# Kernel tuning notes

Hardware: AMD Instinct MI355X
Metric: run time of the kernel (lower is better)

Reference implementation:

```python
import jax, jax.numpy as jnp
import numpy as np

B, T, V, C = 4, 2048, 1024, 256
NB_L, NB_M, NB_H = 16, 32, 64


def _band_w(basis, coeffs, soft):
    # basis: (V, 2*nb), coeffs: (C, 2*nb) -> w: (V, C)
    w = basis @ coeffs.T
    return jax.nn.softmax(w, axis=0) if soft else w


def _rms_norm(x):
    eps = jnp.asarray(jnp.finfo(x.dtype).eps, x.dtype)
    return x * jax.lax.rsqrt(jnp.mean(jnp.square(x), axis=-1, keepdims=True) + eps)


def _retrieve(x, basis, qc, kc, vc, decay_logit):
    # x: (B,T,V) -> (B,T,C); decay-weighted dense T x T retrieval
    q = x @ _band_w(basis, qc, True)
    k = x @ _band_w(basis, kc, True)
    v = x @ _band_w(basis, vc, True)
    scores = jnp.einsum('btc,bsc->bts', q, k)
    decay = jax.nn.sigmoid(decay_logit)
    pos = jnp.arange(T)
    diff = pos[None, :] - pos[:, None]  # diff[i,j] = j - i (as in torch code)
    dw = (decay ** jnp.maximum(diff - 1, 0).astype(x.dtype)) * (diff > 0).astype(x.dtype)
    return jnp.einsum('bts,bsc->btc', scores * dw[None], v)


def _project(r, basis, oc, out_scale):
    return jnp.einsum('btc,vc->btv', r, basis @ oc.T) * out_scale


def _transform(x, basis, read_c, mix, bias):
    z = x @ _band_w(basis, read_c, True)
    return jax.nn.gelu(z @ mix + bias, approximate=False)


def _write_back(h, basis, write_c, out_scale):
    return jnp.einsum('btc,vc->btv', h, basis @ write_c.T) * out_scale


def setup_inputs() -> dict:
    key = jax.random.key(0)
    ks = iter(jax.random.split(key, 48))
    s = 0.02

    def rn(shape, scale=s):
        return jax.random.normal(next(ks), shape, dtype=jnp.float32) * scale

    d = {
        'x': jax.random.normal(next(ks), (B, T, V), dtype=jnp.float32),
        'basis_low': jax.random.normal(next(ks), (V, 2 * NB_L), dtype=jnp.float32),
        'basis_mid': jax.random.normal(next(ks), (V, 2 * NB_M), dtype=jnp.float32),
        'basis_high': jax.random.normal(next(ks), (V, 2 * NB_H), dtype=jnp.float32),
    }
    for pre, nb, dec in (('slow', NB_L, 4.0), ('fast', NB_H, 2.0)):
        for nm in ('q', 'k', 'v', 'o'):
            d[f'{pre}_{nm}'] = rn((C, 2 * nb))
        d[f'{pre}_decay'] = jnp.asarray(dec, jnp.float32)
        d[f'{pre}_scale'] = jnp.asarray(0.1, jnp.float32)
    for pre, nb in (('low', NB_L), ('mid', NB_M), ('high', NB_H)):
        d[f'{pre}_read'] = rn((C, 2 * nb))
        d[f'{pre}_write'] = rn((C, 2 * nb))
        d[f'{pre}_mix'] = rn((C, C))
        d[f'{pre}_bias'] = jnp.zeros((C,), jnp.float32)
        d[f'{pre}_oscale'] = jnp.asarray(0.1, jnp.float32)
    d['tg_w'] = rn((C, C)); d['tg_b'] = jnp.zeros((C,), jnp.float32)
    d['alpha_w'] = rn((C, C)); d['alpha_b'] = jnp.zeros((C,), jnp.float32)
    for nm in ('mem_slow_scale', 'mem_fast_scale', 'op_low_scale', 'op_mid_scale', 'op_high_scale'):
        d[nm] = jnp.ones((1,), jnp.float32)
    return d


def reference(x, basis_low, basis_mid, basis_high,
              slow_q, slow_k, slow_v, slow_o, slow_decay, slow_scale,
              fast_q, fast_k, fast_v, fast_o, fast_decay, fast_scale,
              low_read, low_write, low_mix, low_bias, low_oscale,
              mid_read, mid_write, mid_mix, mid_bias, mid_oscale,
              high_read, high_write, high_mix, high_bias, high_oscale,
              tg_w, tg_b, alpha_w, alpha_b,
              mem_slow_scale, mem_fast_scale, op_low_scale, op_mid_scale, op_high_scale):
    # Phase 1: temporal mixing
    xn = _rms_norm(x)
    r_slow = _retrieve(xn, basis_low, slow_q, slow_k, slow_v, slow_decay)
    r_fast = _retrieve(xn, basis_high, fast_q, fast_k, fast_v, fast_decay)
    tg = jax.nn.sigmoid(r_slow @ tg_w + tg_b)
    r_fast = tg * r_fast
    x = x + (_project(r_slow, basis_low, slow_o, slow_scale) * mem_slow_scale
             + _project(r_fast, basis_high, fast_o, fast_scale) * mem_fast_scale)
    # Phase 2: band processing
    xn = _rms_norm(x)
    h_low = _transform(xn, basis_low, low_read, low_mix, low_bias)
    h_mid = _transform(xn, basis_mid, mid_read, mid_mix, mid_bias)
    h_high = _transform(xn, basis_high, high_read, high_mix, high_bias)
    ag = jax.nn.sigmoid(h_low @ alpha_w + alpha_b)
    h_high = ag * h_high
    x = x + (_write_back(h_low, basis_low, low_write, low_oscale) * op_low_scale
             + _write_back(h_mid, basis_mid, mid_write, mid_oscale) * op_mid_scale
             + _write_back(h_high, basis_high, high_write, high_oscale) * op_high_scale)
    return x
```

## Files before the change

kernel.cpp:

```cpp
#include <hip/hip_runtime.h>
#include <math.h>

#define BB 4
#define TT 2048
#define VV 1024
#define CC 256
#define MR (BB*TT)

using short8  = __attribute__((ext_vector_type(8))) short;
using ushort8 = __attribute__((ext_vector_type(8))) unsigned short;
using f32x4   = __attribute__((ext_vector_type(4))) float;

__device__ __forceinline__ float bs2f(unsigned short s) {
    return __uint_as_float(((unsigned int)s) << 16);
}
__device__ __forceinline__ unsigned short f2bs(float f) {
    unsigned int u = __float_as_uint(f);
    u += 0x7fffu + ((u >> 16) & 1u);
    return (unsigned short)(u >> 16);
}
__device__ __forceinline__ void gl_lds16(const void* g, void* l) {
    __builtin_amdgcn_global_load_lds(
        (const __attribute__((address_space(1))) unsigned int*)g,
        (__attribute__((address_space(3))) unsigned int*)l, 16, 0, 0);
}
__device__ __forceinline__ float sigm(float x) { return 1.f / (1.f + expf(-x)); }
__device__ __forceinline__ float erf_f(float x) {
    float ax = fabsf(x);
    float t = 1.f / (1.f + 0.3275911f * ax);
    float p = t * (0.254829592f + t * (-0.284496736f + t * (1.421413741f +
              t * (-1.453152027f + t * 1.061405429f))));
    float e = 1.f - p * expf(-ax * ax);
    return copysignf(e, x);
}

struct CastJob { const float* src; unsigned short* dst; int n; };
struct CastArgs { CastJob j[17]; };

__global__ void cast_bf16_multi(CastArgs a) {
    CastJob jb = a.j[blockIdx.x];
    int off = (blockIdx.y * 256 + threadIdx.x) * 8;
    if (off + 8 > jb.n) return;
    float4 v0 = *reinterpret_cast<const float4*>(jb.src + off);
    float4 v1 = *reinterpret_cast<const float4*>(jb.src + off + 4);
    ushort8 u;
    u[0] = f2bs(v0.x); u[1] = f2bs(v0.y); u[2] = f2bs(v0.z); u[3] = f2bs(v0.w);
    u[4] = f2bs(v1.x); u[5] = f2bs(v1.y); u[6] = f2bs(v1.z); u[7] = f2bs(v1.w);
    *reinterpret_cast<ushort8*>(jb.dst + off) = u;
}

__global__ void softmax_rows(unsigned short* __restrict__ w) {
    int row = blockIdx.x * 4 + (threadIdx.x >> 6);
    int lane = threadIdx.x & 63;
    ushort4* rp = reinterpret_cast<ushort4*>(w + (size_t)row * 1024);
    float v[16];
    #pragma unroll
    for (int i = 0; i < 4; ++i) {
        ushort4 u = rp[lane + i * 64];
        v[i*4+0] = bs2f(u.x); v[i*4+1] = bs2f(u.y);
        v[i*4+2] = bs2f(u.z); v[i*4+3] = bs2f(u.w);
    }
    float m = v[0];
    #pragma unroll
    for (int i = 1; i < 16; ++i) m = fmaxf(m, v[i]);
    #pragma unroll
    for (int o = 32; o > 0; o >>= 1) m = fmaxf(m, __shfl_xor(m, o));
    float s = 0.f;
    #pragma unroll
    for (int i = 0; i < 16; ++i) { v[i] = expf(v[i] - m); s += v[i]; }
    #pragma unroll
    for (int o = 32; o > 0; o >>= 1) s += __shfl_xor(s, o);
    float inv = 1.f / s;
    #pragma unroll
    for (int i = 0; i < 4; ++i) {
        ushort4 u;
        u.x = f2bs(v[i*4+0] * inv); u.y = f2bs(v[i*4+1] * inv);
        u.z = f2bs(v[i*4+2] * inv); u.w = f2bs(v[i*4+3] * inv);
        rp[lane + i * 64] = u;
    }
}

__global__ void prep_T5(const float* s0, const float* s1, const float* s2,
                        const float* s3, const float* s4,
                        unsigned short* d0, unsigned short* d1, unsigned short* d2,
                        unsigned short* d3, unsigned short* d4) {
    int y = blockIdx.y;
    const float* W = y == 0 ? s0 : y == 1 ? s1 : y == 2 ? s2 : y == 3 ? s3 : s4;
    unsigned short* WT = y == 0 ? d0 : y == 1 ? d1 : y == 2 ? d2 : y == 3 ? d3 : d4;
    int n = blockIdx.x, k = threadIdx.x;
    WT[(size_t)n * 256 + k] = f2bs(W[(size_t)k * 256 + n]);
}

__global__ void rmsnorm_k(const float* __restrict__ x, unsigned short* __restrict__ xn) {
    int row = blockIdx.x * 4 + (threadIdx.x >> 6);
    int lane = threadIdx.x & 63;
    const float4* src = reinterpret_cast<const float4*>(x + (size_t)row * VV);
    float4 v[4];
    float s = 0.f;
    #pragma unroll
    for (int i = 0; i < 4; ++i) {
        v[i] = src[lane + i * 64];
        s += v[i].x*v[i].x + v[i].y*v[i].y + v[i].z*v[i].z + v[i].w*v[i].w;
    }
    #pragma unroll
    for (int o = 32; o > 0; o >>= 1) s += __shfl_xor(s, o);
    float r = rsqrtf(s * (1.f / VV) + 1.1920929e-7f);
    ushort4* dst = reinterpret_cast<ushort4*>(xn + (size_t)row * VV);
    #pragma unroll
    for (int i = 0; i < 4; ++i) {
        ushort4 u;
        u.x = f2bs(v[i].x * r); u.y = f2bs(v[i].y * r);
        u.z = f2bs(v[i].z * r); u.w = f2bs(v[i].w * r);
        dst[lane + i * 64] = u;
    }
}

__global__ void transpose4_k(const unsigned short* __restrict__ qkv,
                             unsigned short* __restrict__ vt_s,
                             unsigned short* __restrict__ vt_f,
                             unsigned short* __restrict__ kts_s,
                             unsigned short* __restrict__ kts_f,
                             const float* __restrict__ dls,
                             const float* __restrict__ dlf) {
    __shared__ unsigned short tile[32][33];
    int z = blockIdx.z, b = z & 3, which = z >> 2;
    int srcoff = which == 0 ? 512 : which == 1 ? 1280 : which == 2 ? 256 : 1024;
    unsigned short* dst = which == 0 ? vt_s : which == 1 ? vt_f : which == 2 ? kts_s : kts_f;
    float l2d = 0.f;
    if (which == 2) l2d = log2f(sigm(dls[0]));
    if (which == 3) l2d = log2f(sigm(dlf[0]));
    int t0 = blockIdx.x * 32, c0 = blockIdx.y * 32;
    int tx = threadIdx.x & 31, ty = threadIdx.x >> 5;
    const unsigned short* src = qkv + srcoff;
    #pragma unroll
    for (int i = 0; i < 4; ++i) {
        int r = ty + i * 8;
        tile[r][tx] = src[(size_t)(b * TT + t0 + r) * 1536 + c0 + tx];
    }
    __syncthreads();
    float w = (which >= 2) ? exp2f(l2d * (float)((t0 + tx) & 127)) : 1.f;
    #pragma unroll
    for (int i = 0; i < 4; ++i) {
        int r = ty + i * 8;
        dst[((size_t)b * CC + c0 + r) * TT + t0 + tx] = f2bs(bs2f(tile[tx][r]) * w);
    }
}

__device__ __forceinline__ void gemm64_core(
    const unsigned short* A, int lda, const unsigned short* Bt, int ldb,
    int K, int m0, int n0, short8* As, short8* Bs, f32x4 (&acc)[2][2]) {
    const int tid = threadIdx.x;
    const int lane = tid & 63, wid = tid >> 6;
    const int wm = wid >> 1, wn = wid & 1;
    const int lrow = tid >> 2, lch = tid & 3;
    const int sws = lch ^ ((lrow >> 1) & 3);
    const unsigned short* ag = A + (size_t)(m0 + lrow) * lda + lch * 8;
    const unsigned short* bg = Bt + (size_t)(n0 + lrow) * ldb + lch * 8;
    #pragma unroll
    for (int i = 0; i < 2; ++i)
        #pragma unroll
        for (int j = 0; j < 2; ++j) acc[i][j] = {0.f, 0.f, 0.f, 0.f};
    const int g = lane >> 4;
    const int ra0 = wm * 32 + (lane & 15);
    const int rb0 = wn * 32 + (lane & 15);
    for (int k0 = 0; k0 < K; k0 += 32) {
        As[lrow * 4 + sws] = *reinterpret_cast<const short8*>(ag + k0);
        Bs[lrow * 4 + sws] = *reinterpret_cast<const short8*>(bg + k0);
        __syncthreads();
        short8 af[2], bf[2];
        #pragma unroll
        for (int i = 0; i < 2; ++i) {
            int ra = ra0 + i * 16;
            af[i] = As[ra * 4 + (g ^ ((ra >> 1) & 3))];
            int rb = rb0 + i * 16;
            bf[i] = Bs[rb * 4 + (g ^ ((rb >> 1) & 3))];
        }
        #pragma unroll
        for (int i = 0; i < 2; ++i)
            #pragma unroll
            for (int j = 0; j < 2; ++j)
                acc[i][j] = __builtin_amdgcn_mfma_f32_16x16x32_bf16(af[i], bf[j], acc[i][j], 0, 0, 0);
        __syncthreads();
    }
}

#define EPI_LOOP(MV, NV, VV_, BODY)                                            \
    {   const int lane_ = threadIdx.x & 63, wid_ = threadIdx.x >> 6;           \
        const int wm_ = wid_ >> 1, wn_ = wid_ & 1;                             \
        _Pragma("unroll")                                                      \
        for (int i_ = 0; i_ < 2; ++i_)                                         \
        { _Pragma("unroll")                                                    \
          for (int j_ = 0; j_ < 2; ++j_)                                       \
          { _Pragma("unroll")                                                  \
            for (int r_ = 0; r_ < 4; ++r_)                                     \
            { int MV = m0 + wm_ * 32 + i_ * 16 + (lane_ >> 4) * 4 + r_;        \
              int NV = n0 + wn_ * 32 + j_ * 16 + (lane_ & 15);                 \
              float VV_ = acc[i_][j_][r_];                                     \
              BODY } } } }

struct MJob {
    const unsigned short* A; const unsigned short* Bt; unsigned short* outb;
    const float* s1; const float* s2;
    int lda, ldb, K, ldo, gx, nblk;
};
struct MJobs5 { MJob j[5]; };

template<int EPI>
__global__ __launch_bounds__(256)
void gemm_multi_k(MJobs5 js) {
    int bid = blockIdx.x, ji = 0, base = 0;
    while (bid >= base + js.j[ji].nblk) { base += js.j[ji].nblk; ++ji; }
    MJob jb = js.j[ji];
    int rem = bid - base;
    int m0 = (rem / jb.gx) * 64, n0 = (rem % jb.gx) * 64;
    __shared__ short8 As[256], Bs[256];
    f32x4 acc[2][2];
    gemm64_core(jb.A, jb.lda, jb.Bt, jb.ldb, jb.K, m0, n0, As, Bs, acc);
    float sc = 1.f;
    if constexpr (EPI == 4) sc = jb.s1[0] * jb.s2[0];
    EPI_LOOP(m, n, v, { jb.outb[(size_t)m * jb.ldo + n] = f2bs(v * sc); })
}

__global__ __launch_bounds__(256)
void sig_k(const unsigned short* A, int lda, const unsigned short* Bt,
           const float* bias, const unsigned short* aux, int ldaux,
           unsigned short* outb, int ldo, int coloff) {
    int m0 = blockIdx.y * 64, n0 = blockIdx.x * 64;
    __shared__ short8 As[256], Bs[256];
    f32x4 acc[2][2];
    gemm64_core(A, lda, Bt, 256, 256, m0, n0, As, Bs, acc);
    EPI_LOOP(m, n, v, {
        float s = sigm(v + bias[n]);
        float a = bs2f(aux[(size_t)m * ldaux + n]);
        outb[(size_t)m * ldo + coloff + n] = f2bs(s * a);
    })
}

__global__ __launch_bounds__(256)
void gelu3_k(const unsigned short* zbuf, const unsigned short* WT_mix,
             const float* lb, const float* mb, const float* hb,
             unsigned short* hcat, unsigned short* hhigh) {
    int zi = blockIdx.z;
    const unsigned short* A = zbuf + zi * 256;
    const unsigned short* Bt = WT_mix + (size_t)zi * 65536;
    const float* bias = zi == 0 ? lb : zi == 1 ? mb : hb;
    unsigned short* outb = zi == 2 ? hhigh : hcat;
    int ldo = zi == 2 ? 256 : 768;
    int coloff = zi == 1 ? 256 : 0;
    int m0 = blockIdx.y * 64, n0 = blockIdx.x * 64;
    __shared__ short8 As[256], Bs[256];
    f32x4 acc[2][2];
    gemm64_core(A, 768, Bt, 256, 256, m0, n0, As, Bs, acc);
    EPI_LOOP(m, n, v, {
        float z = v + bias[n];
        float h = 0.5f * z * (1.f + erf_f(z * 0.70710678118654752f));
        outb[(size_t)m * ldo + coloff + n] = f2bs(h);
    })
}

__global__ __launch_bounds__(256)
void gstate_k(const unsigned short* kts_s, const unsigned short* vt_s,
              const unsigned short* kts_f, const unsigned short* vt_f,
              float* Gs, float* Gf) {
    int zz = blockIdx.z;
    int sel = zz >> 6, z2 = zz & 63;
    int zb = z2 >> 4, zp = z2 & 15;
    const unsigned short* A  = (sel ? vt_f  : vt_s)  + (size_t)(zb * CC) * TT + zp * 128;
    const unsigned short* Bt = (sel ? kts_f : kts_s) + (size_t)(zb * CC) * TT + zp * 128;
    float* G = (sel ? Gf : Gs) + (size_t)z2 * 65536;
    int m0 = blockIdx.y * 64, n0 = blockIdx.x * 64;
    __shared__ short8 As[256], Bs[256];
    f32x4 acc[2][2];
    gemm64_core(A, TT, Bt, TT, 128, m0, n0, As, Bs, acc);
    EPI_LOOP(m, n, v, { G[(size_t)m * 256 + n] = v; })
}

__global__ __launch_bounds__(256)
void inter_k(const unsigned short* qkv,
             const unsigned short* ST_s, const unsigned short* ST_f,
             const float* dls, const float* dlf,
             unsigned short* rcat, unsigned short* rfast) {
    int zz = blockIdx.z;
    int sel = zz >= 60, z2 = sel ? zz - 60 : zz;
    int zb = z2 / 15, zp = z2 % 15;
    const unsigned short* A = qkv + (sel ? 768 : 0) + (size_t)(zb * TT + zp * 128) * 1536;
    const unsigned short* Bt = (sel ? ST_f : ST_s) + (size_t)z2 * 65536;
    unsigned short* outb = sel ? rfast : rcat;
    int ldo = sel ? 256 : 512;
    float l2d = log2f(sigm(sel ? dlf[0] : dls[0]));
    int m0 = blockIdx.y * 64, n0 = blockIdx.x * 64;
    __shared__ short8 As[256], Bs[256];
    f32x4 acc[2][2];
    gemm64_core(A, 1536, Bt, 256, 256, m0, n0, As, Bs, acc);
    EPI_LOOP(m, n, v, {
        float rs = exp2f(l2d * (float)(127 - m));
        size_t idx = (size_t)(zb * TT + zp * 128 + m) * ldo + n;
        outb[idx] = f2bs(bs2f(outb[idx]) + v * rs);
    })
}

struct EpiP {
    float* outf; const float* addf;
    unsigned short* outb; int ldo;
};

template<int EPI>
__global__ __launch_bounds__(256)
void gemm128_k(const unsigned short* __restrict__ A, int lda,
               const unsigned short* __restrict__ Bt, int ldb, int K, EpiP ep) {
    __shared__ short8 As[1024], Bs[1024];
    const int tid = threadIdx.x;
    const int lane = tid & 63, wid = tid >> 6;
    const int wm = wid >> 1, wn = wid & 1;

    int lin = blockIdx.y * gridDim.x + blockIdx.x;
    int ngw = gridDim.x * gridDim.y;
    int q8 = ngw >> 3;
    int sw = (lin & 7) * q8 + (lin >> 3);
    const int m0 = (sw / gridDim.x) * 128, n0 = (sw % gridDim.x) * 128;

    const int srow = lane >> 3, schk = (lane & 7) ^ srow;
    const unsigned short* ga = A + (size_t)(m0 + wid * 32 + srow) * lda + schk * 8;
    const unsigned short* gb = Bt + (size_t)(n0 + wid * 32 + srow) * ldb + schk * 8;
    short8* lA = &As[(wid * 32) * 8];
    short8* lB = &Bs[(wid * 32) * 8];

    const int fr = lane & 15, fg = lane >> 4;

    f32x4 acc[4][4];
    #pragma unroll
    for (int i = 0; i < 4; ++i)
        #pragma unroll
        for (int j = 0; j < 4; ++j) acc[i][j] = {0.f, 0.f, 0.f, 0.f};

    for (int k0 = 0; k0 < K; k0 += 64) {
        #pragma unroll
        for (int q = 0; q < 4; ++q) {
            gl_lds16(ga + (size_t)(q * 8) * lda + k0, lA + q * 64);
            gl_lds16(gb + (size_t)(q * 8) * ldb + k0, lB + q * 64);
        }
        __syncthreads();
        #pragma unroll
        for (int kk = 0; kk < 2; ++kk) {
            short8 af[4], bf[4];
            #pragma unroll
            for (int i = 0; i < 4; ++i) {
                int ra = wm * 64 + i * 16 + fr;
                af[i] = As[ra * 8 + ((kk * 4 + fg) ^ (ra & 7))];
                int rb = wn * 64 + i * 16 + fr;
                bf[i] = Bs[rb * 8 + ((kk * 4 + fg) ^ (rb & 7))];
            }
            #pragma unroll
            for (int i = 0; i < 4; ++i)
                #pragma unroll
                for (int j = 0; j < 4; ++j)
                    acc[i][j] = __builtin_amdgcn_mfma_f32_16x16x32_bf16(af[i], bf[j], acc[i][j], 0, 0, 0);
        }
        __syncthreads();
    }

    #pragma unroll
    for (int i = 0; i < 4; ++i) {
        #pragma unroll
        for (int j = 0; j < 4; ++j) {
            #pragma unroll
            for (int r = 0; r < 4; ++r) {
                int m = m0 + wm * 64 + i * 16 + fg * 4 + r;
                int n = n0 + wn * 64 + j * 16 + fr;
                float v = acc[i][j][r];
                if constexpr (EPI == 0) {
                    ep.outb[(size_t)m * ep.ldo + n] = f2bs(v);
                } else {
                    size_t idx = (size_t)m * ep.ldo + n;
                    ep.outf[idx] = ep.addf[idx] + v;
                }
            }
        }
    }
}

__global__ __launch_bounds__(256)
void attn_k(const unsigned short* __restrict__ qkv,
            const unsigned short* __restrict__ vt_s,
            const unsigned short* __restrict__ vt_f,
            const float* __restrict__ dls, const float* __restrict__ dlf,
            unsigned short* __restrict__ rcat, unsigned short* __restrict__ rfast) {
    int y = blockIdx.y;
    int qoff = y ? 768 : 0, koff = y ? 1024 : 256;
    const unsigned short* vt = y ? vt_f : vt_s;
    unsigned short* rout = y ? rfast : rcat;
    int ldr = y ? 256 : 512;
    float l2d = log2f(sigm(y ? dlf[0] : dls[0]));

    int blk = blockIdx.x;
    int b = blk >> 7;
    int t0 = (blk & 127) << 4;
    int tid = threadIdx.x;
    int lane = tid & 63, wid = tid >> 6;

    __shared__ short8 Pl[4][64];
    __shared__ float  red[16][260];

    short8 qf[8];
    const size_t rowq = (size_t)(b * TT + t0 + (lane & 15)) * 1536 + qoff + (lane >> 4) * 8;
    #pragma unroll
    for (int ch = 0; ch < 8; ++ch)
        qf[ch] = *reinterpret_cast<const short8*>(qkv + rowq + ch * 32);

    f32x4 racc[16];
    #pragma unroll
    for (int i = 0; i < 16; ++i) racc[i] = {0.f, 0.f, 0.f, 0.f};

    unsigned short* pb = reinterpret_cast<unsigned short*>(&Pl[wid][0]);

    int sBeg = t0 & ~31;
    int sEnd = (t0 & ~127) + 128;
    const int tl = (lane >> 4) * 4;

    for (int s0 = sBeg + wid * 32; s0 < sEnd; s0 += 128) {
        #pragma unroll
        for (int h = 0; h < 2; ++h) {
            f32x4 sacc = {0.f, 0.f, 0.f, 0.f};
            const unsigned short* kb =
                qkv + (size_t)(b * TT + s0 + h * 16 + (lane & 15)) * 1536 + koff + (lane >> 4) * 8;
            #pragma unroll
            for (int ch = 0; ch < 8; ++ch) {
                short8 kf = *reinterpret_cast<const short8*>(kb + ch * 32);
                sacc = __builtin_amdgcn_mfma_f32_16x16x32_bf16(qf[ch], kf, sacc, 0, 0, 0);
            }
            int scol = s0 + h * 16 + (lane & 15);
            #pragma unroll
            for (int r = 0; r < 4; ++r) {
                int trow = t0 + tl + r;
                int d = scol - trow;
                float w = (d > 0) ? exp2f(l2d * (float)(d - 1)) : 0.f;
                int prow = tl + r, pcol = h * 16 + (lane & 15);
                int swp = (pcol >> 3) ^ ((prow >> 1) & 3);
                pb[(prow * 4 + swp) * 8 + (pcol & 7)] = f2bs(sacc[r] * w);
            }
        }
        asm volatile("s_waitcnt lgkmcnt(0)" ::: "memory");
        __builtin_amdgcn_sched_barrier(0);
        short8 pf;
        { int prow = lane & 15; pf = Pl[wid][prow * 4 + ((lane >> 4) ^ ((prow >> 1) & 3))]; }
        const unsigned short* vb = vt + ((size_t)b * CC + (lane & 15)) * TT + s0 + (lane >> 4) * 8;
        #pragma unroll
        for (int nt = 0; nt < 16; ++nt) {
            short8 vf = *reinterpret_cast<const short8*>(vb + (size_t)nt * 16 * TT);
            racc[nt] = __builtin_amdgcn_mfma_f32_16x16x32_bf16(pf, vf, racc[nt], 0, 0, 0);
        }
    }

    for (int w = 0; w < 4; ++w) {
        if (wid == w) {
            #pragma unroll
            for (int nt = 0; nt < 16; ++nt)
                #pragma unroll
                for (int r = 0; r < 4; ++r) {
                    int row = tl + r, col = nt * 16 + (lane & 15);
                    if (w == 0) red[row][col] = racc[nt][r];
                    else        red[row][col] += racc[nt][r];
                }
        }
        __syncthreads();
    }

    {
        int row = tid >> 4, c0 = (tid & 15) * 16;
        ushort8 lo, hi;
        #pragma unroll
        for (int j = 0; j < 8; ++j) lo[j] = f2bs(red[row][c0 + j]);
        #pragma unroll
        for (int j = 0; j < 8; ++j) hi[j] = f2bs(red[row][c0 + 8 + j]);
        unsigned short* dst = rout + (size_t)(b * TT + t0 + row) * ldr + c0;
        *reinterpret_cast<ushort8*>(dst)     = lo;
        *reinterpret_cast<ushort8*>(dst + 8) = hi;
    }
}

__global__ void scan_states2(const float* __restrict__ Gs, const float* __restrict__ Gf,
                             const float* __restrict__ dls, const float* __restrict__ dlf,
                             unsigned short* __restrict__ STs, unsigned short* __restrict__ STf) {
    int sel = blockIdx.z;
    const float* G = sel ? Gf : Gs;
    unsigned short* ST = sel ? STf : STs;
    float d = sigm(sel ? dlf[0] : dls[0]);
    int b = blockIdx.y;
    int e0 = (blockIdx.x * 256 + threadIdx.x) * 4;
    float dL = exp2f(log2f(d) * 128.f);
    float4 s = {0.f, 0.f, 0.f, 0.f};
    for (int c = 15; c >= 1; --c) {
        float4 g = *reinterpret_cast<const float4*>(G + (((size_t)(b * 16 + c)) << 16) + e0);
        s.x = g.x + dL * s.x; s.y = g.y + dL * s.y;
        s.z = g.z + dL * s.z; s.w = g.w + dL * s.w;
        ushort4 o;
        o.x = f2bs(s.x); o.y = f2bs(s.y); o.z = f2bs(s.z); o.w = f2bs(s.w);
        *reinterpret_cast<ushort4*>(ST + (((size_t)(b * 15 + c - 1)) << 16) + e0) = o;
    }
}

extern "C" void kernel_launch(void* const* d_in, const int* in_sizes, int n_in,
                              void* d_out, int out_size, void* d_ws, size_t ws_size,
                              hipStream_t stream) {
    (void)in_sizes; (void)n_in; (void)out_size; (void)ws_size;
    const float* x          = (const float*)d_in[0];
    const float* basis_low  = (const float*)d_in[1];
    const float* basis_mid  = (const float*)d_in[2];
    const float* basis_high = (const float*)d_in[3];
    const float* slow_q = (const float*)d_in[4];
    const float* slow_k = (const float*)d_in[5];
    const float* slow_v = (const float*)d_in[6];
    const float* slow_o = (const float*)d_in[7];
    const float* slow_decay = (const float*)d_in[8];
    const float* slow_scale = (const float*)d_in[9];
    const float* fast_q = (const float*)d_in[10];
    const float* fast_k = (const float*)d_in[11];
    const float* fast_v = (const float*)d_in[12];
    const float* fast_o = (const float*)d_in[13];
    const float* fast_decay = (const float*)d_in[14];
    const float* fast_scale = (const float*)d_in[15];
    const float* low_read  = (const float*)d_in[16];
    const float* low_write = (const float*)d_in[17];
    const float* low_mix   = (const float*)d_in[18];
    const float* low_bias  = (const float*)d_in[19];
    const float* low_oscale= (const float*)d_in[20];
    const float* mid_read  = (const float*)d_in[21];
    const float* mid_write = (const float*)d_in[22];
    const float* mid_mix   = (const float*)d_in[23];
    const float* mid_bias  = (const float*)d_in[24];
    const float* mid_oscale= (const float*)d_in[25];
    const float* high_read  = (const float*)d_in[26];
    const float* high_write = (const float*)d_in[27];
    const float* high_mix   = (const float*)d_in[28];
    const float* high_bias  = (const float*)d_in[29];
    const float* high_oscale= (const float*)d_in[30];
    const float* tg_w    = (const float*)d_in[31];
    const float* tg_b    = (const float*)d_in[32];
    const float* alpha_w = (const float*)d_in[33];
    const float* alpha_b = (const float*)d_in[34];
    const float* mem_slow_scale = (const float*)d_in[35];
    const float* mem_fast_scale = (const float*)d_in[36];
    const float* op_low_scale   = (const float*)d_in[37];
    const float* op_mid_scale   = (const float*)d_in[38];
    const float* op_high_scale  = (const float*)d_in[39];
    float* out = (float*)d_out;

    char* ws = (char*)d_ws;
    size_t off = 0;
    auto alloc = [&](size_t n) { char* p = ws + off; off += (n + 255) & ~(size_t)255; return p; };
    unsigned short* WT_p1   = (unsigned short*)alloc((size_t)6 * CC * VV * 2);
    unsigned short* WT_read = (unsigned short*)alloc((size_t)3 * CC * VV * 2);
    unsigned short* Wcat_o  = (unsigned short*)alloc((size_t)VV * 512 * 2);
    unsigned short* Wcat_w  = (unsigned short*)alloc((size_t)VV * 768 * 2);
    unsigned short* WT_mix  = (unsigned short*)alloc((size_t)3 * 65536 * 2);
    unsigned short* WT_tg   = (unsigned short*)alloc((size_t)65536 * 2);
    unsigned short* WT_al   = (unsigned short*)alloc((size_t)65536 * 2);
    unsigned short* bb_low  = (unsigned short*)alloc((size_t)VV * 32 * 2);
    unsigned short* bb_mid  = (unsigned short*)alloc((size_t)VV * 64 * 2);
    unsigned short* bb_high = (unsigned short*)alloc((size_t)VV * 128 * 2);
    unsigned short* cqkv_l  = (unsigned short*)alloc((size_t)768 * 32 * 2);
    unsigned short* cqkv_h  = (unsigned short*)alloc((size_t)768 * 128 * 2);
    unsigned short* crd_l   = (unsigned short*)alloc((size_t)256 * 32 * 2);
    unsigned short* crd_m   = (unsigned short*)alloc((size_t)256 * 64 * 2);
    unsigned short* crd_h   = (unsigned short*)alloc((size_t)256 * 128 * 2);
    unsigned short* cO_s    = (unsigned short*)alloc((size_t)256 * 32 * 2);
    unsigned short* cO_f    = (unsigned short*)alloc((size_t)256 * 128 * 2);
    unsigned short* cW_l    = (unsigned short*)alloc((size_t)256 * 32 * 2);
    unsigned short* cW_m    = (unsigned short*)alloc((size_t)256 * 64 * 2);
    unsigned short* cW_h    = (unsigned short*)alloc((size_t)256 * 128 * 2);
    unsigned short* xn      = (unsigned short*)alloc((size_t)MR * VV * 2);
    unsigned short* qkv     = (unsigned short*)alloc((size_t)MR * 1536 * 2);
    unsigned short* vt_s    = (unsigned short*)alloc((size_t)BB * CC * TT * 2);
    unsigned short* vt_f    = (unsigned short*)alloc((size_t)BB * CC * TT * 2);
    unsigned short* kts_s   = (unsigned short*)alloc((size_t)BB * CC * TT * 2);
    unsigned short* kts_f   = (unsigned short*)alloc((size_t)BB * CC * TT * 2);
    unsigned short* ST_s    = (unsigned short*)alloc((size_t)BB * 15 * 65536 * 2);
    unsigned short* ST_f    = (unsigned short*)alloc((size_t)BB * 15 * 65536 * 2);
    unsigned short* rcat    = (unsigned short*)alloc((size_t)MR * 512 * 2);
    unsigned short* rfast   = (unsigned short*)alloc((size_t)MR * CC * 2);
    unsigned short* hhigh   = (unsigned short*)alloc((size_t)MR * CC * 2);
    float* Gs = (float*)xn;
    float* Gf = (float*)rcat;
    unsigned short* z    = qkv;
    unsigned short* hcat = qkv + (size_t)MR * 768;

    {
        CastArgs ca;
        int i = 0;
        auto J = [&](const float* s, unsigned short* d, int n) { ca.j[i].src = s; ca.j[i].dst = d; ca.j[i].n = n; ++i; };
        J(basis_low,  bb_low,  VV * 32);
        J(basis_mid,  bb_mid,  VV * 64);
        J(basis_high, bb_high, VV * 128);
        J(slow_q, cqkv_l + 0 * 256 * 32, 256 * 32);
        J(slow_k, cqkv_l + 1 * 256 * 32, 256 * 32);
        J(slow_v, cqkv_l + 2 * 256 * 32, 256 * 32);
        J(fast_q, cqkv_h + 0 * 256 * 128, 256 * 128);
        J(fast_k, cqkv_h + 1 * 256 * 128, 256 * 128);
        J(fast_v, cqkv_h + 2 * 256 * 128, 256 * 128);
        J(low_read,  crd_l, 256 * 32);
        J(mid_read,  crd_m, 256 * 64);
        J(high_read, crd_h, 256 * 128);
        J(slow_o,    cO_s,  256 * 32);
        J(fast_o,    cO_f,  256 * 128);
        J(low_write, cW_l,  256 * 32);
        J(mid_write, cW_m,  256 * 64);
        J(high_write,cW_h,  256 * 128);
        cast_bf16_multi<<<dim3(17, 64), 256, 0, stream>>>(ca);
    }

    {
        MJobs5 js;
        auto S = [&](int i, const unsigned short* A, int lda, const unsigned short* B, int K,
                     unsigned short* o, int nb) {
            js.j[i].A = A; js.j[i].Bt = B; js.j[i].outb = o; js.j[i].s1 = nullptr; js.j[i].s2 = nullptr;
            js.j[i].lda = lda; js.j[i].ldb = K; js.j[i].K = K; js.j[i].ldo = VV; js.j[i].gx = 16; js.j[i].nblk = nb;
        };
        S(0, cqkv_l, 32,  bb_low,  32,  WT_p1,                    192);
        S(1, cqkv_h, 128, bb_high, 128, WT_p1 + (size_t)768 * VV, 192);
        S(2, crd_l,  32,  bb_low,  32,  WT_read,                   64);
        S(3, crd_m,  64,  bb_mid,  64,  WT_read + (size_t)256 * VV, 64);
        S(4, crd_h,  128, bb_high, 128, WT_read + (size_t)512 * VV, 64);
        gemm_multi_k<0><<<576, 256, 0, stream>>>(js);
    }
    softmax_rows<<<576, 256, 0, stream>>>(WT_p1);

    {
        MJobs5 js;
        auto S = [&](int i, const unsigned short* A, int lda, const unsigned short* B, int K,
                     unsigned short* o, int ldo, const float* s1, const float* s2) {
            js.j[i].A = A; js.j[i].Bt = B; js.j[i].outb = o; js.j[i].s1 = s1; js.j[i].s2 = s2;
            js.j[i].lda = lda; js.j[i].ldb = K; js.j[i].K = K; js.j[i].ldo = ldo; js.j[i].gx = 4; js.j[i].nblk = 64;
        };
        S(0, bb_low,  32,  cO_s, 32,  Wcat_o,       512, slow_scale,  mem_slow_scale);
        S(1, bb_high, 128, cO_f, 128, Wcat_o + 256, 512, fast_scale,  mem_fast_scale);
        S(2, bb_low,  32,  cW_l, 32,  Wcat_w,       768, low_oscale,  op_low_scale);
        S(3, bb_mid,  64,  cW_m, 64,  Wcat_w + 256, 768, mid_oscale,  op_mid_scale);
        S(4, bb_high, 128, cW_h, 128, Wcat_w + 512, 768, high_oscale, op_high_scale);
        gemm_multi_k<4><<<320, 256, 0, stream>>>(js);
    }

    prep_T5<<<dim3(256, 5), 256, 0, stream>>>(tg_w, alpha_w, low_mix, mid_mix, high_mix,
                                              WT_tg, WT_al, WT_mix, WT_mix + 65536, WT_mix + 131072);

    rmsnorm_k<<<MR / 4, 256, 0, stream>>>(x, xn);
    { EpiP ep{}; ep.outb = qkv; ep.ldo = 1536;
      gemm128_k<0><<<dim3(12, 64), 256, 0, stream>>>(xn, 1024, WT_p1, 1024, 1024, ep); }
    transpose4_k<<<dim3(64, 8, 16), 256, 0, stream>>>(qkv, vt_s, vt_f, kts_s, kts_f, slow_decay, fast_decay);
    gstate_k<<<dim3(4, 4, 128), 256, 0, stream>>>(kts_s, vt_s, kts_f, vt_f, Gs, Gf);
    scan_states2<<<dim3(64, 4, 2), 256, 0, stream>>>(Gs, Gf, slow_decay, fast_decay, ST_s, ST_f);
    attn_k<<<dim3(512, 2), 256, 0, stream>>>(qkv, vt_s, vt_f, slow_decay, fast_decay, rcat, rfast);
    inter_k<<<dim3(4, 2, 120), 256, 0, stream>>>(qkv, ST_s, ST_f, slow_decay, fast_decay, rcat, rfast);
    sig_k<<<dim3(4, 128), 256, 0, stream>>>(rcat, 512, WT_tg, tg_b, rfast, 256, rcat, 512, 256);
    { EpiP ep{}; ep.outf = out; ep.addf = x; ep.ldo = 1024;
      gemm128_k<3><<<dim3(8, 64), 256, 0, stream>>>(rcat, 512, Wcat_o, 512, 512, ep); }

    rmsnorm_k<<<MR / 4, 256, 0, stream>>>(out, xn);
    { EpiP ep{}; ep.outb = z; ep.ldo = 768;
      gemm128_k<0><<<dim3(6, 64), 256, 0, stream>>>(xn, 1024, WT_read, 1024, 1024, ep); }
    gelu3_k<<<dim3(4, 128, 3), 256, 0, stream>>>(z, WT_mix, low_bias, mid_bias, high_bias, hcat, hhigh);
    sig_k<<<dim3(4, 128), 256, 0, stream>>>(hcat, 768, WT_al, alpha_b, hhigh, 256, hcat, 768, 512);
    { EpiP ep{}; ep.outf = out; ep.addf = out; ep.ldo = 1024;
      gemm128_k<3><<<dim3(6, 64), 256, 0, stream>>>(hcat, 768, Wcat_w, 768, 768, ep); }
}
```

Before: 274.4 us.

## Double-buffer gemm128 K-loop with BK=32 and reuse it for chunk-state GEMM

Rewrites the 128x128 GEMM main loop to use two LDS buffers with a K step of 32. The next tile is prefetched via global_load_lds while the current one feeds MFMAs, using vmcnt waits and raw s_barriers instead of two __syncthreads per iteration. The separate 64x64 gstate kernel is replaced by a batched instantiation of gemm128 (grid z selects slow/fast and batch/chunk), and the grid swizzle now falls back to linear order when the tile count is not a multiple of 8. The costs are a new swizzle pattern, twice as many loop iterations, and fewer blocks for the state GEMM.

```diff
diff --git a/kernel.cpp b/kernel.cpp
--- a/kernel.cpp
+++ b/kernel.cpp
@@ -256,23 +256,6 @@
         float h = 0.5f * z * (1.f + erf_f(z * 0.70710678118654752f));
         outb[(size_t)m * ldo + coloff + n] = f2bs(h);
     })
-}
-
-__global__ __launch_bounds__(256)
-void gstate_k(const unsigned short* kts_s, const unsigned short* vt_s,
-              const unsigned short* kts_f, const unsigned short* vt_f,
-              float* Gs, float* Gf) {
-    int zz = blockIdx.z;
-    int sel = zz >> 6, z2 = zz & 63;
-    int zb = z2 >> 4, zp = z2 & 15;
-    const unsigned short* A  = (sel ? vt_f  : vt_s)  + (size_t)(zb * CC) * TT + zp * 128;
-    const unsigned short* Bt = (sel ? kts_f : kts_s) + (size_t)(zb * CC) * TT + zp * 128;
-    float* G = (sel ? Gf : Gs) + (size_t)z2 * 65536;
-    int m0 = blockIdx.y * 64, n0 = blockIdx.x * 64;
-    __shared__ short8 As[256], Bs[256];
-    f32x4 acc[2][2];
-    gemm64_core(A, TT, Bt, TT, 128, m0, n0, As, Bs, acc);
-    EPI_LOOP(m, n, v, { G[(size_t)m * 256 + n] = v; })
 }
 
 __global__ __launch_bounds__(256)
@@ -302,28 +285,37 @@
 struct EpiP {
     float* outf; const float* addf;
     unsigned short* outb; int ldo;
+    const unsigned short* A2; const unsigned short* B2;
+    float* outf2;
 };
 
-template<int EPI>
+template<int EPI, int BATCH>
 __global__ __launch_bounds__(256)
 void gemm128_k(const unsigned short* __restrict__ A, int lda,
                const unsigned short* __restrict__ Bt, int ldb, int K, EpiP ep) {
-    __shared__ short8 As[1024], Bs[1024];
+    __shared__ short8 As[2][512], Bs[2][512];
     const int tid = threadIdx.x;
     const int lane = tid & 63, wid = tid >> 6;
     const int wm = wid >> 1, wn = wid & 1;
 
+    int sel = 0, z2v = 0;
+    if constexpr (BATCH == 1) {
+        int zz = blockIdx.z; sel = zz >> 6; z2v = zz & 63;
+        int zb = z2v >> 4, zp = z2v & 15;
+        if (sel) { A = ep.A2; Bt = ep.B2; }
+        A  += (size_t)(zb * CC) * lda + zp * 128;
+        Bt += (size_t)(zb * CC) * ldb + zp * 128;
+    }
+
     int lin = blockIdx.y * gridDim.x + blockIdx.x;
     int ngw = gridDim.x * gridDim.y;
-    int q8 = ngw >> 3;
-    int sw = (lin & 7) * q8 + (lin >> 3);
+    int sw = lin;
+    if (!(ngw & 7)) sw = (lin & 7) * (ngw >> 3) + (lin >> 3);
     const int m0 = (sw / gridDim.x) * 128, n0 = (sw % gridDim.x) * 128;
 
-    const int srow = lane >> 3, schk = (lane & 7) ^ srow;
+    const int srow = lane >> 2, schk = (lane & 3) ^ ((srow >> 1) & 3);
     const unsigned short* ga = A + (size_t)(m0 + wid * 32 + srow) * lda + schk * 8;
     const unsigned short* gb = Bt + (size_t)(n0 + wid * 32 + srow) * ldb + schk * 8;
-    short8* lA = &As[(wid * 32) * 8];
-    short8* lB = &Bs[(wid * 32) * 8];
 
     const int fr = lane & 15, fg = lane >> 4;
 
@@ -333,31 +325,46 @@
         #pragma unroll
         for (int j = 0; j < 4; ++j) acc[i][j] = {0.f, 0.f, 0.f, 0.f};
 
-    for (int k0 = 0; k0 < K; k0 += 64) {
-        #pragma unroll
-        for (int q = 0; q < 4; ++q) {
-            gl_lds16(ga + (size_t)(q * 8) * lda + k0, lA + q * 64);
-            gl_lds16(gb + (size_t)(q * 8) * ldb + k0, lB + q * 64);
+    auto stage = [&](int buf, int k0) {
+        short8* lA = &As[buf][(wid * 32) * 4];
+        short8* lB = &Bs[buf][(wid * 32) * 4];
+        gl_lds16(ga + k0, lA);
+        gl_lds16(ga + (size_t)16 * lda + k0, lA + 64);
+        gl_lds16(gb + k0, lB);
+        gl_lds16(gb + (size_t)16 * ldb + k0, lB + 64);
+    };
+
+    stage(0, 0);
+    int cur = 0;
+    for (int k0 = 0; k0 < K; k0 += 32) {
+        if (k0 + 32 < K) {
+            stage(cur ^ 1, k0 + 32);
+            asm volatile("s_waitcnt vmcnt(4)" ::: "memory");
+        } else {
+            asm volatile("s_waitcnt vmcnt(0)" ::: "memory");
         }
-        __syncthreads();
-        #pragma unroll
-        for (int kk = 0; kk < 2; ++kk) {
-            short8 af[4], bf[4];
+        __builtin_amdgcn_s_barrier();
+        __builtin_amdgcn_sched_barrier(0);
+        short8 af[4], bf[4];
+        #pragma unroll
+        for (int i = 0; i < 4; ++i) {
+            int ra = wm * 64 + i * 16 + fr;
+            af[i] = As[cur][ra * 4 + (fg ^ ((ra >> 1) & 3))];
+            int rb = wn * 64 + i * 16 + fr;
+            bf[i] = Bs[cur][rb * 4 + (fg ^ ((rb >> 1) & 3))];
+        }
+        #pragma unroll
+        for (int i = 0; i < 4; ++i)
             #pragma unroll
-            for (int i = 0; i < 4; ++i) {
-                int ra = wm * 64 + i * 16 + fr;
-                af[i] = As[ra * 8 + ((kk * 4 + fg) ^ (ra & 7))];
-                int rb = wn * 64 + i * 16 + fr;
-                bf[i] = Bs[rb * 8 + ((kk * 4 + fg) ^ (rb & 7))];
-            }
-            #pragma unroll
-            for (int i = 0; i < 4; ++i)
-                #pragma unroll
-                for (int j = 0; j < 4; ++j)
-                    acc[i][j] = __builtin_amdgcn_mfma_f32_16x16x32_bf16(af[i], bf[j], acc[i][j], 0, 0, 0);
-        }
-        __syncthreads();
-    }
+            for (int j = 0; j < 4; ++j)
+                acc[i][j] = __builtin_amdgcn_mfma_f32_16x16x32_bf16(af[i], bf[j], acc[i][j], 0, 0, 0);
+        __builtin_amdgcn_sched_barrier(0);
+        __builtin_amdgcn_s_barrier();
+        cur ^= 1;
+    }
+
+    float* gout = nullptr;
+    if constexpr (EPI == 5) gout = (sel ? ep.outf2 : ep.outf) + (size_t)z2v * 65536;
 
     #pragma unroll
     for (int i = 0; i < 4; ++i) {
@@ -370,9 +377,11 @@
                 float v = acc[i][j][r];
                 if constexpr (EPI == 0) {
                     ep.outb[(size_t)m * ep.ldo + n] = f2bs(v);
-                } else {
+                } else if constexpr (EPI == 3) {
                     size_t idx = (size_t)m * ep.ldo + n;
                     ep.outf[idx] = ep.addf[idx] + v;
+                } else {
+                    gout[(size_t)m * 256 + n] = v;
                 }
             }
         }
@@ -644,21 +653,22 @@
 
     rmsnorm_k<<<MR / 4, 256, 0, stream>>>(x, xn);
     { EpiP ep{}; ep.outb = qkv; ep.ldo = 1536;
-      gemm128_k<0><<<dim3(12, 64), 256, 0, stream>>>(xn, 1024, WT_p1, 1024, 1024, ep); }
+      gemm128_k<0,0><<<dim3(12, 64), 256, 0, stream>>>(xn, 1024, WT_p1, 1024, 1024, ep); }
     transpose4_k<<<dim3(64, 8, 16), 256, 0, stream>>>(qkv, vt_s, vt_f, kts_s, kts_f, slow_decay, fast_decay);
-    gstate_k<<<dim3(4, 4, 128), 256, 0, stream>>>(kts_s, vt_s, kts_f, vt_f, Gs, Gf);
+    { EpiP ep{}; ep.outf = Gs; ep.outf2 = Gf; ep.A2 = vt_f; ep.B2 = kts_f;
+      gemm128_k<5,1><<<dim3(2, 2, 128), 256, 0, stream>>>(vt_s, TT, kts_s, TT, 128, ep); }
     scan_states2<<<dim3(64, 4, 2), 256, 0, stream>>>(Gs, Gf, slow_decay, fast_decay, ST_s, ST_f);
     attn_k<<<dim3(512, 2), 256, 0, stream>>>(qkv, vt_s, vt_f, slow_decay, fast_decay, rcat, rfast);
     inter_k<<<dim3(4, 2, 120), 256, 0, stream>>>(qkv, ST_s, ST_f, slow_decay, fast_decay, rcat, rfast);
     sig_k<<<dim3(4, 128), 256, 0, stream>>>(rcat, 512, WT_tg, tg_b, rfast, 256, rcat, 512, 256);
     { EpiP ep{}; ep.outf = out; ep.addf = x; ep.ldo = 1024;
-      gemm128_k<3><<<dim3(8, 64), 256, 0, stream>>>(rcat, 512, Wcat_o, 512, 512, ep); }
+      gemm128_k<3,0><<<dim3(8, 64), 256, 0, stream>>>(rcat, 512, Wcat_o, 512, 512, ep); }
 
     rmsnorm_k<<<MR / 4, 256, 0, stream>>>(out, xn);
     { EpiP ep{}; ep.outb = z; ep.ldo = 768;
-      gemm128_k<0><<<dim3(6, 64), 256, 0, stream>>>(xn, 1024, WT_read, 1024, 1024, ep); }
+      gemm128_k<0,0><<<dim3(6, 64), 256, 0, stream>>>(xn, 1024, WT_read, 1024, 1024, ep); }
     gelu3_k<<<dim3(4, 128, 3), 256, 0, stream>>>(z, WT_mix, low_bias, mid_bias, high_bias, hcat, hhigh);
     sig_k<<<dim3(4, 128), 256, 0, stream>>>(hcat, 768, WT_al, alpha_b, hhigh, 256, hcat, 768, 512);
     { EpiP ep{}; ep.outf = out; ep.addf = out; ep.ldo = 1024;
-      gemm128_k<3><<<dim3(6, 64), 256, 0, stream>>>(hcat, 768, Wcat_w, 768, 768, ep); }
-}
+      gemm128_k<3,0><<<dim3(6, 64), 256, 0, stream>>>(hcat, 768, Wcat_w, 768, 768, ep); }
+}
```

Result: no change. 277.6 us (+1.2%).
